# Kernel tuning notes

Hardware: AMD Instinct MI355X
Metric: run time of the kernel (lower is better)

The kernel has to match this reference:

```python
import jax, jax.numpy as jnp
import numpy as np

B, N, D, NS, HID, ITERS = 32, 4096, 256, 8, 128, 3
EPS = 1e-8
LN_EPS = 1e-5


def _ln(x, g, b):
    mu = jnp.mean(x, axis=-1, keepdims=True)
    var = jnp.mean(jnp.square(x - mu), axis=-1, keepdims=True)
    return (x - mu) * jax.lax.rsqrt(var + LN_EPS) * g + b


def setup_inputs() -> dict:
    key = jax.random.key(0)
    ks = jax.random.split(key, 32)
    scale = D ** -0.5

    def lin(k, out_d, in_d):
        return jax.random.normal(k, (out_d, in_d), jnp.float32) * (in_d ** -0.5)

    inp = {
        "inputs": jax.random.normal(ks[0], (B, N, D), jnp.float32),
        "slot_noise": jax.random.normal(ks[1], (B, NS, D), jnp.float32),
        "slots_mu": jax.random.uniform(ks[2], (1, 1, D), jnp.float32, -1.0, 1.0) * scale,
        "slots_sigma": jax.random.uniform(ks[3], (1, 1, D), jnp.float32, -1.0, 1.0) * scale,
        "Wq": lin(ks[4], D, D),
        "Wk": lin(ks[5], D, D),
        "Wv": lin(ks[6], D, D),
        "gru_w_ih": lin(ks[7], 3 * D, 2 * D),
        "gru_w_hh": lin(ks[8], 3 * D, D),
        "gru_b_ih": jnp.zeros((3 * D,), jnp.float32),
        "gru_b_hh": jnp.zeros((3 * D,), jnp.float32),
        "obj_w1": lin(ks[9], HID, D),
        "obj_b1": jnp.zeros((HID,), jnp.float32),
        "obj_w2": lin(ks[10], D, HID),
        "obj_b2": jnp.zeros((D,), jnp.float32),
        "rel_w1": lin(ks[11], HID, 2 * D),
        "rel_b1": jnp.zeros((HID,), jnp.float32),
        "rel_w2": lin(ks[12], D, HID),
        "rel_b2": jnp.zeros((D,), jnp.float32),
        "ln_in_g": jnp.ones((D,), jnp.float32),
        "ln_in_b": jnp.zeros((D,), jnp.float32),
        "ln_s_g": jnp.ones((D,), jnp.float32),
        "ln_s_b": jnp.zeros((D,), jnp.float32),
        "ln_ff_g": jnp.ones((D,), jnp.float32),
        "ln_ff_b": jnp.zeros((D,), jnp.float32),
    }
    return inp


def _rel_msg(x, rel_w1, rel_b1, rel_w2, rel_b2):
    # x: (b, n_s, d). rel_mlp(cat(x_i, x_j)) without materializing the concat:
    # split first layer weight into the x_i and x_j halves.
    A = rel_w1[:, :D]   # (hid, d)
    Bm = rel_w1[:, D:]  # (hid, d)
    xa = jnp.einsum('bid,hd->bih', x, A)
    xb = jnp.einsum('bjd,hd->bjh', x, Bm)
    h = jax.nn.relu(xa[:, :, None, :] + xb[:, None, :, :] + rel_b1)  # (b,ns,ns,hid)
    msg = jnp.einsum('bijh,dh->bijd', h, rel_w2) + rel_b2            # (b,ns,ns,d)
    n_s = x.shape[1]
    diag = jnp.eye(n_s, dtype=bool)[None, :, :, None]
    msg = jnp.where(diag, 0.0, msg)
    return msg.sum(axis=2) / (n_s - 1)


def _gru_cell(x, h, w_ih, w_hh, b_ih, b_hh):
    gx = x @ w_ih.T + b_ih  # (B*, 3d)
    gh = h @ w_hh.T + b_hh
    xr, xz, xn = jnp.split(gx, 3, axis=-1)
    hr, hz, hn = jnp.split(gh, 3, axis=-1)
    r = jax.nn.sigmoid(xr + hr)
    z = jax.nn.sigmoid(xz + hz)
    n = jnp.tanh(xn + r * hn)
    return (1.0 - z) * n + z * h


def reference(inputs, slot_noise, slots_mu, slots_sigma, Wq, Wk, Wv,
              gru_w_ih, gru_w_hh, gru_b_ih, gru_b_hh,
              obj_w1, obj_b1, obj_w2, obj_b2,
              rel_w1, rel_b1, rel_w2, rel_b2,
              ln_in_g, ln_in_b, ln_s_g, ln_s_b, ln_ff_g, ln_ff_b):
    b, n, d = inputs.shape
    n_s = slot_noise.shape[1]
    scale = d ** -0.5

    slots = slots_mu + slot_noise * jnp.exp(slots_sigma)  # (b, n_s, d)

    x = _ln(inputs, ln_in_g, ln_in_b)
    k = jnp.einsum('bnd,ed->bne', x, Wk)
    v = jnp.einsum('bnd,ed->bne', x, Wv)

    attns = []
    for _ in range(ITERS):
        slots_prev = slots
        q = jnp.einsum('bid,ed->bie', _ln(slots, ln_s_g, ln_s_b), Wq)
        dots = jnp.einsum('bid,bjd->bij', q, k) * scale        # (b, n_s, n)
        attn = jax.nn.softmax(dots, axis=1) + EPS              # softmax over slots
        attns.append(attn)
        attn_n = attn / attn.sum(axis=-1, keepdims=True)
        updates = jnp.einsum('bjd,bij->bid', v, attn_n)        # (b, n_s, d)
        rel = _rel_msg(slots_prev, rel_w1, rel_b1, rel_w2, rel_b2)
        gin = jnp.concatenate([updates, rel], axis=-1).reshape(b * n_s, 2 * d)
        slots = _gru_cell(gin, slots_prev.reshape(b * n_s, d),
                          gru_w_ih, gru_w_hh, gru_b_ih, gru_b_hh).reshape(b, n_s, d)
        ff = _ln(slots, ln_ff_g, ln_ff_b)
        slots = slots + (jax.nn.relu(ff @ obj_w1.T + obj_b1) @ obj_w2.T + obj_b2)
    return slots, jnp.stack(attns)
```

## Files before the change

kernel.cpp:

```cpp
#include <hip/hip_runtime.h>
#include <hip/hip_bf16.h>
#include <math.h>

static constexpr int Bc   = 32;
static constexpr int Nc   = 4096;
static constexpr int Dc   = 256;
static constexpr int NSc  = 8;
static constexpr int HIDc = 128;
static constexpr int ITERSc = 3;
#define EPSf 1e-8f
#define LN_EPSf 1e-5f

typedef __attribute__((ext_vector_type(8))) short bf16x8;
typedef __attribute__((ext_vector_type(8))) unsigned short u16x8;
typedef __attribute__((ext_vector_type(4))) float f32x4;

static constexpr int W1AT = 0;
static constexpr int W1BT = 32768;
static constexpr int W2T  = 65536;
static constexpr int OW1T = 98304;
static constexpr int OW2T = 131072;
static constexpr int WHNT = 163840;
static constexpr int TW_ELEMS = 229376;

__device__ __forceinline__ float bf2f(unsigned int u) {
  return __uint_as_float((u & 0xffffu) << 16);
}

__device__ __forceinline__ unsigned short f2bfu(float f) {
  unsigned int u = __float_as_uint(f);
  unsigned int r = (u + 0x7fffu + ((u >> 16) & 1u)) >> 16;
  return (unsigned short)r;
}

__device__ __forceinline__ void gl_lds16(const void* g, void* l) {
  __builtin_amdgcn_global_load_lds(
      (__attribute__((address_space(1))) void*)(g),
      (__attribute__((address_space(3))) void*)(l), 16, 0, 0);
}

__device__ __forceinline__ float block_sum(float v, float* tmp) {
  #pragma unroll
  for (int o = 32; o > 0; o >>= 1) v += __shfl_down(v, o, 64);
  int lane = threadIdx.x & 63, wid = threadIdx.x >> 6;
  __syncthreads();
  if (lane == 0) tmp[wid] = v;
  __syncthreads();
  return tmp[0] + tmp[1] + tmp[2] + tmp[3];
}

__device__ __forceinline__ float sigmf(float x) { return 1.f / (1.f + expf(-x)); }

__global__ __launch_bounds__(256) void k_init_slots(const float* __restrict__ noise,
                                                    const float* __restrict__ mu,
                                                    const float* __restrict__ sigma,
                                                    float* __restrict__ slots) {
  int idx = blockIdx.x * 256 + threadIdx.x;
  int d = idx & (Dc - 1);
  slots[idx] = mu[d] + noise[idx] * expf(sigma[d]);
}

__global__ __launch_bounds__(256) void k_lnx(const float* __restrict__ inp,
                                             const float* __restrict__ lng,
                                             const float* __restrict__ lnb,
                                             unsigned short* __restrict__ X) {
  __shared__ float smu[16], srs[16];
  int t = threadIdx.x, lane = t & 63, w = t >> 6;
  size_t row0 = (size_t)blockIdx.x * 16;
  for (int rr = 0; rr < 4; rr++) {
    int row = w * 4 + rr;
    float4 v = *(const float4*)(inp + (row0 + row) * 256 + lane * 4);
    float s = v.x + v.y + v.z + v.w;
    float q = v.x * v.x + v.y * v.y + v.z * v.z + v.w * v.w;
    #pragma unroll
    for (int o = 32; o > 0; o >>= 1) { s += __shfl_down(s, o, 64); q += __shfl_down(q, o, 64); }
    if (lane == 0) {
      float mu = s * (1.0f / 256.0f);
      smu[row] = mu;
      srs[row] = rsqrtf(q * (1.0f / 256.0f) - mu * mu + LN_EPSf);
    }
  }
  __syncthreads();
  #pragma unroll
  for (int p = 0; p < 2; p++) {
    int idx = p * 256 + t;
    int row = idx >> 5, ch = idx & 31;
    const float* src = inp + (row0 + row) * 256 + ch * 8;
    float mu = smu[row], rs = srs[row];
    float4 x0 = *(const float4*)(src);
    float4 x1 = *(const float4*)(src + 4);
    float4 g0 = *(const float4*)(lng + ch * 8);
    float4 g1 = *(const float4*)(lng + ch * 8 + 4);
    float4 b0 = *(const float4*)(lnb + ch * 8);
    float4 b1 = *(const float4*)(lnb + ch * 8 + 4);
    u16x8 pk;
    pk[0] = f2bfu((x0.x - mu) * rs * g0.x + b0.x);
    pk[1] = f2bfu((x0.y - mu) * rs * g0.y + b0.y);
    pk[2] = f2bfu((x0.z - mu) * rs * g0.z + b0.z);
    pk[3] = f2bfu((x0.w - mu) * rs * g0.w + b0.w);
    pk[4] = f2bfu((x1.x - mu) * rs * g1.x + b1.x);
    pk[5] = f2bfu((x1.y - mu) * rs * g1.y + b1.y);
    pk[6] = f2bfu((x1.z - mu) * rs * g1.z + b1.z);
    pk[7] = f2bfu((x1.w - mu) * rs * g1.w + b1.w);
    *(u16x8*)(X + (row0 + row) * 256 + ch * 8) = pk;
  }
}

__global__ __launch_bounds__(256) void k_wprep(const float* __restrict__ w_ih,
                                               const float* __restrict__ w_hh,
                                               unsigned short* __restrict__ Wcat) {
  int idx = blockIdx.x * 256 + threadIdx.x;
  int o = idx / 768, c = idx - o * 768;
  float v;
  if (c < 512) v = w_ih[o * 512 + c];
  else v = (o < 512) ? w_hh[o * 256 + (c - 512)] : 0.f;
  Wcat[idx] = f2bfu(v);
}

__global__ __launch_bounds__(256) void k_tprep(const float* __restrict__ rel_w1,
                                               const float* __restrict__ rel_w2,
                                               const float* __restrict__ obj_w1,
                                               const float* __restrict__ obj_w2,
                                               const float* __restrict__ w_hh,
                                               unsigned short* __restrict__ Tw) {
  int i = blockIdx.x * 256 + threadIdx.x;
  if (i >= TW_ELEMS) return;
  float v;
  if (i < W1BT) { int j = i - W1AT; int d = j >> 7, h = j & 127; v = rel_w1[h * 512 + d]; }
  else if (i < W2T)  { int j = i - W1BT; int d = j >> 7, h = j & 127; v = rel_w1[h * 512 + 256 + d]; }
  else if (i < OW1T) { int j = i - W2T;  int h = j >> 8, o = j & 255; v = rel_w2[o * 128 + h]; }
  else if (i < OW2T) { int j = i - OW1T; int d = j >> 7, h = j & 127; v = obj_w1[h * 256 + d]; }
  else if (i < WHNT) { int j = i - OW2T; int h = j >> 8, o = j & 255; v = obj_w2[o * 128 + h]; }
  else               { int j = i - WHNT; int d = j >> 8, o = j & 255; v = w_hh[(512 + o) * 256 + d]; }
  Tw[i] = f2bfu(v);
}

__global__ __launch_bounds__(256) void k_mprep(const float* __restrict__ Wk,
                                               const float* __restrict__ Wq,
                                               const float* __restrict__ Wv,
                                               float* __restrict__ MT,
                                               float* __restrict__ WvT) {
  int d = blockIdx.x, t = threadIdx.x;
  float acc = 0.f;
  for (int c = 0; c < 256; c++) acc += Wk[c * 256 + t] * Wq[c * 256 + d];
  MT[d * 256 + t] = acc;
  WvT[d * 256 + t] = Wv[t * 256 + d];
}

__global__ __launch_bounds__(256) void k_qproj0(const float* __restrict__ slots,
                                                const float* __restrict__ MT,
                                                const float* __restrict__ g,
                                                const float* __restrict__ bb_,
                                                unsigned short* __restrict__ qkb,
                                                float* __restrict__ S,
                                                float* __restrict__ updraw) {
  __shared__ float xs[Dc];
  __shared__ float tmp[4];
  int t = threadIdx.x;
  int row = blockIdx.x;
  updraw[row * 256 + t] = 0.f;
  if (blockIdx.x == 0) S[t] = 0.f;
  float x = slots[row * Dc + t];
  float s = block_sum(x, tmp);
  float m = s * (1.0f / Dc);
  float dx = x - m;
  float s2 = block_sum(dx * dx, tmp);
  float rs = rsqrtf(s2 * (1.0f / Dc) + LN_EPSf);
  xs[t] = dx * rs * g[t] + bb_[t];
  __syncthreads();
  float acc = 0.f;
  for (int d = 0; d < 256; d++) acc += MT[d * 256 + t] * xs[d];
  int b = row >> 3, i = row & 7;
  qkb[(size_t)(b * 16 + i) * 256 + t] = f2bfu(acc);
  qkb[(size_t)(b * 16 + 8 + i) * 256 + t] = 0;
}

__global__ __launch_bounds__(256) void k_attn(const unsigned short* __restrict__ qkb,
                                              const unsigned short* __restrict__ X,
                                              float* __restrict__ attn,
                                              float* __restrict__ S,
                                              float* __restrict__ updraw) {
  __shared__ unsigned short xs[64 * 256];
  __shared__ float dots[16][68];
  __shared__ float at[8][64];
  __shared__ float parts[2][8][256];
  int t = threadIdx.x, lane = t & 63, w = t >> 6;
  int b = blockIdx.x >> 6, jc = blockIdx.x & 63;
  int j0 = jc * 64;
  #pragma unroll
  for (int c = 0; c < 8; c++) {
    int slot = c * 256 + t;
    int tok = slot >> 5, sl = slot & 31;
    int gc = (sl & 24) | ((sl & 7) ^ (tok & 7));
    gl_lds16((const char*)X + (((size_t)(b * 4096 + j0 + tok)) * 256 + gc * 8) * 2,
             (char*)xs + (size_t)(c * 256 + w * 64) * 16);
  }
  int m = lane & 15, quad = lane >> 4;
  const unsigned short* qrow = qkb + (size_t)(b * 16 + m) * 256;
  __syncthreads();
  f32x4 dacc = {0.f, 0.f, 0.f, 0.f};
  int tokb = w * 16 + m;
  #pragma unroll
  for (int ks = 0; ks < 8; ks++) {
    bf16x8 afr = *(const bf16x8*)(qrow + ks * 32 + quad * 8);
    int kchunk = ks * 4 + quad;
    int slot = (kchunk & 24) | ((kchunk & 7) ^ (tokb & 7));
    bf16x8 bfr = *(const bf16x8*)((const char*)xs + (size_t)tokb * 512 + slot * 16);
    dacc = __builtin_amdgcn_mfma_f32_16x16x32_bf16(afr, bfr, dacc, 0, 0, 0);
  }
  #pragma unroll
  for (int r = 0; r < 4; r++) dots[quad * 4 + r][tokb] = dacc[r];
  __syncthreads();
  if (t < 64) {
    float a[8], mx = -1e30f;
    #pragma unroll
    for (int i = 0; i < 8; i++) { a[i] = dots[i][t] * 0.0625f; mx = fmaxf(mx, a[i]); }
    float sum = 0.f;
    #pragma unroll
    for (int i = 0; i < 8; i++) { a[i] = expf(a[i] - mx); sum += a[i]; }
    float inv = 1.f / sum;
    float* ab = attn + (size_t)b * NSc * Nc;
    #pragma unroll
    for (int i = 0; i < 8; i++) {
      float v = a[i] * inv + EPSf;
      a[i] = v;
      at[i][t] = v;
      ab[i * Nc + j0 + t] = v;
    }
    #pragma unroll
    for (int i = 0; i < 8; i++) {
      float s = a[i];
      #pragma unroll
      for (int o = 32; o > 0; o >>= 1) s += __shfl_down(s, o, 64);
      if (lane == 0) atomicAdd(&S[b * NSc + i], s);
    }
  }
  __syncthreads();
  int dg = t & 127, h = t >> 7;
  float acc[8][2];
  #pragma unroll
  for (int i = 0; i < 8; i++) { acc[i][0] = 0.f; acc[i][1] = 0.f; }
  int kchunk = dg >> 2;
  for (int jj = 0; jj < 32; jj++) {
    int tok = h * 32 + jj;
    int slot = (kchunk & 24) | ((kchunk & 7) ^ (tok & 7));
    unsigned int xv = *(const unsigned int*)((const char*)xs + (size_t)tok * 512 + slot * 16 + (dg & 3) * 4);
    float x0 = bf2f(xv), x1 = bf2f(xv >> 16);
    #pragma unroll
    for (int i = 0; i < 8; i++) {
      float av = at[i][tok];
      acc[i][0] += av * x0;
      acc[i][1] += av * x1;
    }
  }
  #pragma unroll
  for (int i = 0; i < 8; i++)
    *(float2*)&parts[h][i][dg * 2] = make_float2(acc[i][0], acc[i][1]);
  __syncthreads();
  for (int i = 0; i < 8; i++) {
    float val = parts[0][i][t] + parts[1][i][t];
    atomicAdd(&updraw[(size_t)(b * NSc + i) * 256 + t], val);
  }
}

__global__ __launch_bounds__(256) void k_slot_a(const float* __restrict__ slots,
                                                const float* __restrict__ updraw,
                                                const float* __restrict__ S,
                                                const unsigned short* __restrict__ Tw,
                                                const float* __restrict__ WvT,
                                                const float* __restrict__ b1,
                                                const float* __restrict__ b2,
                                                unsigned short* __restrict__ Xb) {
  __shared__ float sp[NSc][256];
  __shared__ float un[4][256];
  __shared__ float xpart[2][12][128];
  __shared__ float xabl[12][128];
  __shared__ float hs[4][128];
  int t = threadIdx.x;
  int b = blockIdx.x >> 1, half = blockIdx.x & 1;
  int i0 = half * 4;
  for (int x = t; x < NSc * 256; x += 256) sp[x >> 8][x & 255] = slots[b * NSc * 256 + x];
  for (int r = 0; r < 4; r++) {
    int grow = b * NSc + i0 + r;
    un[r][t] = updraw[(size_t)grow * 256 + t] / S[grow];
  }
  __syncthreads();
  {
    float av[4] = {0.f, 0.f, 0.f, 0.f};
    for (int d = 0; d < 256; d++) {
      float wv = WvT[d * 256 + t];
      #pragma unroll
      for (int r = 0; r < 4; r++) av[r] += wv * un[r][d];
    }
    for (int r = 0; r < 4; r++) {
      int grow = b * NSc + i0 + r;
      Xb[(size_t)grow * 768 + t] = f2bfu(av[r]);
      Xb[(size_t)grow * 768 + 512 + t] = f2bfu(sp[i0 + r][t]);
    }
  }
  int h = t & 127, dh = t >> 7;
  {
    const unsigned short* wa = Tw + W1AT;
    const unsigned short* wb = Tw + W1BT;
    float accb[8] = {0, 0, 0, 0, 0, 0, 0, 0};
    float acca[4] = {0, 0, 0, 0};
    for (int dd = 0; dd < 128; dd++) {
      int d = dh * 128 + dd;
      float wbv = bf2f(wb[d * 128 + h]);
      float wav = bf2f(wa[d * 128 + h]);
      #pragma unroll
      for (int jj = 0; jj < 8; jj++) accb[jj] += wbv * sp[jj][d];
      #pragma unroll
      for (int r = 0; r < 4; r++) acca[r] += wav * sp[i0 + r][d];
    }
    #pragma unroll
    for (int jj = 0; jj < 8; jj++) xpart[dh][jj][h] = accb[jj];
    #pragma unroll
    for (int r = 0; r < 4; r++) xpart[dh][8 + r][h] = acca[r];
  }
  __syncthreads();
  {
    int g = t >> 7;
    for (int jj = g * 6; jj < g * 6 + 6; jj++)
      xabl[jj][h] = xpart[0][jj][h] + xpart[1][jj][h];
  }
  __syncthreads();
  {
    float bv = b1[h];
    int ig = t >> 7;
    #pragma unroll
    for (int ii = 0; ii < 2; ii++) {
      int il = ig * 2 + ii;
      int ibatch = i0 + il;
      float av = xabl[8 + il][h];
      float s = 0.f;
      #pragma unroll
      for (int jj = 0; jj < NSc; jj++) {
        if (jj == ibatch) continue;
        s += fmaxf(av + xabl[jj][h] + bv, 0.f);
      }
      hs[il][h] = s;
    }
  }
  __syncthreads();
  {
    const unsigned short* w2 = Tw + W2T;
    float am[4] = {0, 0, 0, 0};
    for (int hh = 0; hh < 128; hh++) {
      float wv = bf2f(w2[hh * 256 + t]);
      #pragma unroll
      for (int r = 0; r < 4; r++) am[r] += wv * hs[r][hh];
    }
    float bv2 = b2[t];
    for (int r = 0; r < 4; r++) {
      float rel = am[r] * (1.0f / 7.0f) + bv2;
      Xb[(size_t)(b * NSc + i0 + r) * 768 + 256 + t] = f2bfu(rel);
    }
  }
}

__global__ __launch_bounds__(256) void k_gates(const unsigned short* __restrict__ Xb,
                                               const unsigned short* __restrict__ Wcat,
                                               unsigned short* __restrict__ Yb) {
  __shared__ unsigned short Als[64 * 64];
  __shared__ unsigned short Bls[64 * 64];
  int tid = threadIdx.x;
  int lane = tid & 63, w = tid >> 6;
  int idx16 = lane & 15, quad = lane >> 4;
  int m0 = (blockIdx.x / 12) * 64;
  int n0 = (blockIdx.x % 12) * 64;
  int wm = w & 1, wn = w >> 1;
  f32x4 acc[2][2];
  #pragma unroll
  for (int i = 0; i < 2; i++)
    #pragma unroll
    for (int j = 0; j < 2; j++) acc[i][j] = (f32x4){0.f, 0.f, 0.f, 0.f};

  for (int kt = 0; kt < 12; kt++) {
    int k0 = kt * 64;
    #pragma unroll
    for (int c = 0; c < 2; c++) {
      int idx = (w * 2 + c) * 64 + lane;
      int row = idx >> 3, lc = idx & 7;
      int gc = lc ^ (row & 7);
      gl_lds16((const char*)Xb + (size_t)(m0 + row) * 1536 + k0 * 2 + gc * 16,
               (char*)Als + (size_t)(w * 2 + c) * 1024);
      gl_lds16((const char*)Wcat + (size_t)(n0 + row) * 1536 + k0 * 2 + gc * 16,
               (char*)Bls + (size_t)(w * 2 + c) * 1024);
    }
    __syncthreads();
    #pragma unroll
    for (int ks = 0; ks < 2; ks++) {
      bf16x8 af[2], bfr[2];
      int kchunk = ks * 4 + quad;
      #pragma unroll
      for (int mt = 0; mt < 2; mt++) {
        int row = wm * 32 + mt * 16 + idx16;
        af[mt] = *(const bf16x8*)((const char*)Als + (size_t)(row * 8 + (kchunk ^ (row & 7))) * 16);
      }
      #pragma unroll
      for (int nt = 0; nt < 2; nt++) {
        int row = wn * 32 + nt * 16 + idx16;
        bfr[nt] = *(const bf16x8*)((const char*)Bls + (size_t)(row * 8 + (kchunk ^ (row & 7))) * 16);
      }
      #pragma unroll
      for (int mt = 0; mt < 2; mt++)
        #pragma unroll
        for (int nt = 0; nt < 2; nt++)
          acc[mt][nt] = __builtin_amdgcn_mfma_f32_16x16x32_bf16(af[mt], bfr[nt], acc[mt][nt], 0, 0, 0);
    }
    __syncthreads();
  }
  #pragma unroll
  for (int mt = 0; mt < 2; mt++) {
    #pragma unroll
    for (int nt = 0; nt < 2; nt++) {
      int gm = m0 + wm * 32 + mt * 16 + quad * 4;
      int col = n0 + wn * 32 + nt * 16 + idx16;
      #pragma unroll
      for (int r = 0; r < 4; r++)
        Yb[(size_t)(gm + r) * 768 + col] = f2bfu(acc[mt][nt][r]);
    }
  }
}

__global__ __launch_bounds__(256) void k_slot_c(const unsigned short* __restrict__ Yb,
                                                const unsigned short* __restrict__ Tw,
                                                const float* __restrict__ MT,
                                                const float* __restrict__ b_ih,
                                                const float* __restrict__ b_hh,
                                                float* __restrict__ slots,
                                                const float* __restrict__ ob1,
                                                const float* __restrict__ ob2,
                                                const float* __restrict__ lng,
                                                const float* __restrict__ lnb,
                                                const float* __restrict__ lsg,
                                                const float* __restrict__ lsb,
                                                unsigned short* __restrict__ qkb,
                                                float* __restrict__ updraw,
                                                float* __restrict__ S,
                                                float* __restrict__ outf,
                                                int wfinal) {
  __shared__ float sp4[4][256];
  __shared__ float ffl[4][256];
  __shared__ float h1p[2][4][128];
  __shared__ float h1l[4][128];
  __shared__ float xs2[4][256];
  int t = threadIdx.x;
  int g0 = blockIdx.x * 4;
  for (int x = t; x < 1024; x += 256) sp4[x >> 8][x & 255] = slots[(size_t)g0 * 256 + x];
  __syncthreads();
  float hn[4] = {0, 0, 0, 0};
  {
    const unsigned short* wh = Tw + WHNT;
    for (int d = 0; d < 256; d++) {
      float wv = bf2f(wh[d * 256 + t]);
      #pragma unroll
      for (int r = 0; r < 4; r++) hn[r] += wv * sp4[r][d];
    }
  }
  float bir = b_ih[t], bhr = b_hh[t];
  float biz = b_ih[256 + t], bhz = b_hh[256 + t];
  float bin_ = b_ih[512 + t], bhn = b_hh[512 + t];
  float snew[4];
  #pragma unroll
  for (int r = 0; r < 4; r++) {
    size_t yoff = (size_t)(g0 + r) * 768;
    float yr = bf2f((unsigned int)Yb[yoff + t]);
    float yz = bf2f((unsigned int)Yb[yoff + 256 + t]);
    float yx = bf2f((unsigned int)Yb[yoff + 512 + t]);
    float rg = sigmf(yr + bir + bhr);
    float zg = sigmf(yz + biz + bhz);
    float ng = tanhf(yx + bin_ + rg * (hn[r] + bhn));
    snew[r] = (1.f - zg) * ng + zg * sp4[r][t];
    ffl[r][t] = snew[r];
  }
  __syncthreads();
  {
    int wv = t >> 6, lane = t & 63;
    float4 v = *(const float4*)&ffl[wv][lane * 4];
    float s = v.x + v.y + v.z + v.w;
    float q = v.x * v.x + v.y * v.y + v.z * v.z + v.w * v.w;
    #pragma unroll
    for (int o = 32; o > 0; o >>= 1) { s += __shfl_down(s, o, 64); q += __shfl_down(q, o, 64); }
    s = __shfl(s, 0, 64); q = __shfl(q, 0, 64);
    float mu = s * (1.0f / 256.0f);
    float rs = rsqrtf(q * (1.0f / 256.0f) - mu * mu + LN_EPSf);
    float4 g4 = *(const float4*)&lng[lane * 4];
    float4 b4 = *(const float4*)&lnb[lane * 4];
    float4 o4;
    o4.x = (v.x - mu) * rs * g4.x + b4.x;
    o4.y = (v.y - mu) * rs * g4.y + b4.y;
    o4.z = (v.z - mu) * rs * g4.z + b4.z;
    o4.w = (v.w - mu) * rs * g4.w + b4.w;
    *(float4*)&ffl[wv][lane * 4] = o4;
  }
  __syncthreads();
  {
    const unsigned short* w1 = Tw + OW1T;
    int h = t & 127, dh = t >> 7;
    float a1[4] = {0, 0, 0, 0};
    for (int dd = 0; dd < 128; dd++) {
      int d = dh * 128 + dd;
      float wv = bf2f(w1[d * 128 + h]);
      #pragma unroll
      for (int r = 0; r < 4; r++) a1[r] += wv * ffl[r][d];
    }
    #pragma unroll
    for (int r = 0; r < 4; r++) h1p[dh][r][h] = a1[r];
  }
  __syncthreads();
  {
    int h = t & 127, g = t >> 7;
    float bo = ob1[h];
    #pragma unroll
    for (int rr = 0; rr < 2; rr++) {
      int r = g * 2 + rr;
      h1l[r][h] = fmaxf(h1p[0][r][h] + h1p[1][r][h] + bo, 0.f);
    }
  }
  __syncthreads();
  float res[4];
  {
    const unsigned short* w2 = Tw + OW2T;
    float ao[4] = {0, 0, 0, 0};
    for (int hh = 0; hh < 128; hh++) {
      float wv = bf2f(w2[hh * 256 + t]);
      #pragma unroll
      for (int r = 0; r < 4; r++) ao[r] += wv * h1l[r][hh];
    }
    float bo2 = ob2[t];
    #pragma unroll
    for (int r = 0; r < 4; r++) res[r] = snew[r] + ao[r] + bo2;
  }
  #pragma unroll
  for (int r = 0; r < 4; r++) {
    slots[(size_t)(g0 + r) * 256 + t] = res[r];
    if (wfinal) outf[(size_t)(g0 + r) * 256 + t] = res[r];
    xs2[r][t] = res[r];
  }
  __syncthreads();
  {
    int wv = t >> 6, lane = t & 63;
    float4 v = *(const float4*)&xs2[wv][lane * 4];
    float s = v.x + v.y + v.z + v.w;
    float q = v.x * v.x + v.y * v.y + v.z * v.z + v.w * v.w;
    #pragma unroll
    for (int o = 32; o > 0; o >>= 1) { s += __shfl_down(s, o, 64); q += __shfl_down(q, o, 64); }
    s = __shfl(s, 0, 64); q = __shfl(q, 0, 64);
    float mu = s * (1.0f / 256.0f);
    float rs = rsqrtf(q * (1.0f / 256.0f) - mu * mu + LN_EPSf);
    float4 g4 = *(const float4*)&lsg[lane * 4];
    float4 b4 = *(const float4*)&lsb[lane * 4];
    float4 o4;
    o4.x = (v.x - mu) * rs * g4.x + b4.x;
    o4.y = (v.y - mu) * rs * g4.y + b4.y;
    o4.z = (v.z - mu) * rs * g4.z + b4.z;
    o4.w = (v.w - mu) * rs * g4.w + b4.w;
    *(float4*)&xs2[wv][lane * 4] = o4;
  }
  __syncthreads();
  {
    float aq[4] = {0, 0, 0, 0};
    for (int d = 0; d < 256; d++) {
      float wv = MT[d * 256 + t];
      #pragma unroll
      for (int r = 0; r < 4; r++) aq[r] += wv * xs2[r][d];
    }
    #pragma unroll
    for (int r = 0; r < 4; r++) {
      int grow = g0 + r;
      int b = grow >> 3, i = grow & 7;
      qkb[(size_t)(b * 16 + i) * 256 + t] = f2bfu(aq[r]);
      qkb[(size_t)(b * 16 + 8 + i) * 256 + t] = 0;
    }
  }
  #pragma unroll
  for (int r = 0; r < 4; r++) updraw[(size_t)(g0 + r) * 256 + t] = 0.f;
  if (t < 4) S[g0 + t] = 0.f;
}

extern "C" void kernel_launch(void* const* d_in, const int* in_sizes, int n_in,
                              void* d_out, int out_size, void* d_ws, size_t ws_size,
                              hipStream_t stream) {
  const float* inputs      = (const float*)d_in[0];
  const float* slot_noise  = (const float*)d_in[1];
  const float* slots_mu    = (const float*)d_in[2];
  const float* slots_sigma = (const float*)d_in[3];
  const float* Wq          = (const float*)d_in[4];
  const float* Wk          = (const float*)d_in[5];
  const float* Wv          = (const float*)d_in[6];
  const float* gru_w_ih    = (const float*)d_in[7];
  const float* gru_w_hh    = (const float*)d_in[8];
  const float* gru_b_ih    = (const float*)d_in[9];
  const float* gru_b_hh    = (const float*)d_in[10];
  const float* obj_w1      = (const float*)d_in[11];
  const float* obj_b1      = (const float*)d_in[12];
  const float* obj_w2      = (const float*)d_in[13];
  const float* obj_b2      = (const float*)d_in[14];
  const float* rel_w1      = (const float*)d_in[15];
  const float* rel_b1      = (const float*)d_in[16];
  const float* rel_w2      = (const float*)d_in[17];
  const float* rel_b2      = (const float*)d_in[18];
  const float* ln_in_g     = (const float*)d_in[19];
  const float* ln_in_b     = (const float*)d_in[20];
  const float* ln_s_g      = (const float*)d_in[21];
  const float* ln_s_b      = (const float*)d_in[22];
  const float* ln_ff_g     = (const float*)d_in[23];
  const float* ln_ff_b     = (const float*)d_in[24];

  char* w = (char*)d_ws;
  unsigned short* X    = (unsigned short*)(w);
  float* slots  = (float*)(w + (size_t)67108864);
  float* updraw = (float*)(w + (size_t)67371008);
  float* Sbuf   = (float*)(w + (size_t)67633152);
  unsigned short* Wcat = (unsigned short*)(w + (size_t)67634176);
  unsigned short* Tw   = (unsigned short*)(w + (size_t)68813824);
  unsigned short* Xbuf = (unsigned short*)(w + (size_t)69403648);
  unsigned short* Ybuf = (unsigned short*)(w + (size_t)69796864);
  unsigned short* qkb  = (unsigned short*)(w + (size_t)70190080);
  float* MT  = (float*)(w + (size_t)70452224);
  float* WvT = (float*)(w + (size_t)70714368);

  float* out = (float*)d_out;
  float* attn_base = out + (size_t)Bc * NSc * Dc;

  k_init_slots<<<Bc * NSc * Dc / 256, 256, 0, stream>>>(slot_noise, slots_mu, slots_sigma, slots);
  k_lnx<<<Bc * Nc / 16, 256, 0, stream>>>(inputs, ln_in_g, ln_in_b, X);
  k_wprep<<<768 * 768 / 256, 256, 0, stream>>>(gru_w_ih, gru_w_hh, Wcat);
  k_tprep<<<(TW_ELEMS + 255) / 256, 256, 0, stream>>>(rel_w1, rel_w2, obj_w1, obj_w2, gru_w_hh, Tw);
  k_mprep<<<256, 256, 0, stream>>>(Wk, Wq, Wv, MT, WvT);
  k_qproj0<<<Bc * NSc, 256, 0, stream>>>(slots, MT, ln_s_g, ln_s_b, qkb, Sbuf, updraw);

  for (int it = 0; it < ITERSc; it++) {
    float* attn = attn_base + (size_t)it * Bc * NSc * Nc;
    k_attn<<<Bc * 64, 256, 0, stream>>>(qkb, X, attn, Sbuf, updraw);
    k_slot_a<<<Bc * 2, 256, 0, stream>>>(slots, updraw, Sbuf, Tw, WvT, rel_b1, rel_b2, Xbuf);
    k_gates<<<4 * 12, 256, 0, stream>>>(Xbuf, Wcat, Ybuf);
    k_slot_c<<<64, 256, 0, stream>>>(Ybuf, Tw, MT, gru_b_ih, gru_b_hh, slots,
                                     obj_b1, obj_b2, ln_ff_g, ln_ff_b, ln_s_g, ln_s_b,
                                     qkb, updraw, Sbuf,
                                     out, it == ITERSc - 1 ? 1 : 0);
  }
}
```

Measured before the change: 798.3 us.

## Move attention update product onto MFMA using a pre-transposed bf16 input copy

The LayerNorm kernel now also writes a token-major transposed bf16 copy of the normalized inputs. The attention kernel is rewritten with far fewer, larger blocks: each wave computes dots via MFMA straight from global memory and does the 8-slot softmax with lane shuffles. It then computes the attention-weighted value sum with MFMA against the transposed copy, replacing the scalar LDS accumulation loop. Smaller changes: the padded q buffer is dropped, the zero block of the GRU weight matrix is skipped by splitting it in two, and the MT/WvT matrices are stored in bf16. This costs an extra 64MB transposed write, lower occupancy, and slightly lower precision.

```diff
diff --git a/kernel.cpp b/kernel.cpp
--- a/kernel.cpp
+++ b/kernel.cpp
@@ -63,12 +63,16 @@
 __global__ __launch_bounds__(256) void k_lnx(const float* __restrict__ inp,
                                              const float* __restrict__ lng,
                                              const float* __restrict__ lnb,
-                                             unsigned short* __restrict__ X) {
-  __shared__ float smu[16], srs[16];
+                                             unsigned short* __restrict__ X,
+                                             unsigned short* __restrict__ XT) {
+  __shared__ float smu[64], srs[64];
+  __shared__ unsigned short xt[64][264];
   int t = threadIdx.x, lane = t & 63, w = t >> 6;
-  size_t row0 = (size_t)blockIdx.x * 16;
-  for (int rr = 0; rr < 4; rr++) {
-    int row = w * 4 + rr;
+  int b = blockIdx.x >> 6;
+  int tok0 = (blockIdx.x & 63) * 64;
+  size_t row0 = (size_t)b * 4096 + tok0;
+  for (int rr = 0; rr < 16; rr++) {
+    int row = w * 16 + rr;
     float4 v = *(const float4*)(inp + (row0 + row) * 256 + lane * 4);
     float s = v.x + v.y + v.z + v.w;
     float q = v.x * v.x + v.y * v.y + v.z * v.z + v.w * v.w;
@@ -82,7 +86,7 @@
   }
   __syncthreads();
   #pragma unroll
-  for (int p = 0; p < 2; p++) {
+  for (int p = 0; p < 8; p++) {
     int idx = p * 256 + t;
     int row = idx >> 5, ch = idx & 31;
     const float* src = inp + (row0 + row) * 256 + ch * 8;
@@ -103,18 +107,35 @@
     pk[6] = f2bfu((x1.z - mu) * rs * g1.z + b1.z);
     pk[7] = f2bfu((x1.w - mu) * rs * g1.w + b1.w);
     *(u16x8*)(X + (row0 + row) * 256 + ch * 8) = pk;
+    *(u16x8*)&xt[row][ch * 8] = pk;
+  }
+  __syncthreads();
+  {
+    unsigned short* dst = XT + ((size_t)(b * 256 + t)) * 4096 + tok0;
+    #pragma unroll
+    for (int g = 0; g < 8; g++) {
+      u16x8 o;
+      #pragma unroll
+      for (int u = 0; u < 8; u++) o[u] = xt[g * 8 + u][t];
+      *(u16x8*)(dst + g * 8) = o;
+    }
   }
 }
 
 __global__ __launch_bounds__(256) void k_wprep(const float* __restrict__ w_ih,
                                                const float* __restrict__ w_hh,
-                                               unsigned short* __restrict__ Wcat) {
+                                               unsigned short* __restrict__ Wcat1,
+                                               unsigned short* __restrict__ Wcat2) {
   int idx = blockIdx.x * 256 + threadIdx.x;
-  int o = idx / 768, c = idx - o * 768;
-  float v;
-  if (c < 512) v = w_ih[o * 512 + c];
-  else v = (o < 512) ? w_hh[o * 256 + (c - 512)] : 0.f;
-  Wcat[idx] = f2bfu(v);
+  if (idx < 512 * 768) {
+    int o = idx / 768, c = idx - o * 768;
+    float v = (c < 512) ? w_ih[o * 512 + c] : w_hh[o * 256 + (c - 512)];
+    Wcat1[idx] = f2bfu(v);
+  } else {
+    int j = idx - 512 * 768;
+    int o = j >> 9, c = j & 511;
+    Wcat2[j] = f2bfu(w_ih[(512 + o) * 512 + c]);
+  }
 }
 
 __global__ __launch_bounds__(256) void k_tprep(const float* __restrict__ rel_w1,
@@ -138,17 +159,17 @@
 __global__ __launch_bounds__(256) void k_mprep(const float* __restrict__ Wk,
                                                const float* __restrict__ Wq,
                                                const float* __restrict__ Wv,
-                                               float* __restrict__ MT,
-                                               float* __restrict__ WvT) {
+                                               unsigned short* __restrict__ MTb,
+                                               unsigned short* __restrict__ WvTb) {
   int d = blockIdx.x, t = threadIdx.x;
   float acc = 0.f;
   for (int c = 0; c < 256; c++) acc += Wk[c * 256 + t] * Wq[c * 256 + d];
-  MT[d * 256 + t] = acc;
-  WvT[d * 256 + t] = Wv[t * 256 + d];
+  MTb[d * 256 + t] = f2bfu(acc);
+  WvTb[d * 256 + t] = f2bfu(Wv[t * 256 + d]);
 }
 
 __global__ __launch_bounds__(256) void k_qproj0(const float* __restrict__ slots,
-                                                const float* __restrict__ MT,
+                                                const unsigned short* __restrict__ MTb,
                                                 const float* __restrict__ g,
                                                 const float* __restrict__ bb_,
                                                 unsigned short* __restrict__ qkb,
@@ -169,97 +190,104 @@
   xs[t] = dx * rs * g[t] + bb_[t];
   __syncthreads();
   float acc = 0.f;
-  for (int d = 0; d < 256; d++) acc += MT[d * 256 + t] * xs[d];
-  int b = row >> 3, i = row & 7;
-  qkb[(size_t)(b * 16 + i) * 256 + t] = f2bfu(acc);
-  qkb[(size_t)(b * 16 + 8 + i) * 256 + t] = 0;
+  for (int d = 0; d < 256; d++) acc += bf2f(MTb[d * 256 + t]) * xs[d];
+  qkb[(size_t)row * 256 + t] = f2bfu(acc);
 }
 
 __global__ __launch_bounds__(256) void k_attn(const unsigned short* __restrict__ qkb,
                                               const unsigned short* __restrict__ X,
+                                              const unsigned short* __restrict__ XT,
                                               float* __restrict__ attn,
                                               float* __restrict__ S,
                                               float* __restrict__ updraw) {
-  __shared__ unsigned short xs[64 * 256];
-  __shared__ float dots[16][68];
-  __shared__ float at[8][64];
-  __shared__ float parts[2][8][256];
+  __shared__ unsigned short at_bf[4][16][136];
+  __shared__ float updw[4][8][256];
   int t = threadIdx.x, lane = t & 63, w = t >> 6;
-  int b = blockIdx.x >> 6, jc = blockIdx.x & 63;
-  int j0 = jc * 64;
-  #pragma unroll
-  for (int c = 0; c < 8; c++) {
-    int slot = c * 256 + t;
-    int tok = slot >> 5, sl = slot & 31;
-    int gc = (sl & 24) | ((sl & 7) ^ (tok & 7));
-    gl_lds16((const char*)X + (((size_t)(b * 4096 + j0 + tok)) * 256 + gc * 8) * 2,
-             (char*)xs + (size_t)(c * 256 + w * 64) * 16);
-  }
-  int m = lane & 15, quad = lane >> 4;
-  const unsigned short* qrow = qkb + (size_t)(b * 16 + m) * 256;
-  __syncthreads();
-  f32x4 dacc = {0.f, 0.f, 0.f, 0.f};
-  int tokb = w * 16 + m;
-  #pragma unroll
-  for (int ks = 0; ks < 8; ks++) {
-    bf16x8 afr = *(const bf16x8*)(qrow + ks * 32 + quad * 8);
-    int kchunk = ks * 4 + quad;
-    int slot = (kchunk & 24) | ((kchunk & 7) ^ (tokb & 7));
-    bf16x8 bfr = *(const bf16x8*)((const char*)xs + (size_t)tokb * 512 + slot * 16);
-    dacc = __builtin_amdgcn_mfma_f32_16x16x32_bf16(afr, bfr, dacc, 0, 0, 0);
-  }
-  #pragma unroll
-  for (int r = 0; r < 4; r++) dots[quad * 4 + r][tokb] = dacc[r];
-  __syncthreads();
-  if (t < 64) {
-    float a[8], mx = -1e30f;
-    #pragma unroll
-    for (int i = 0; i < 8; i++) { a[i] = dots[i][t] * 0.0625f; mx = fmaxf(mx, a[i]); }
-    float sum = 0.f;
-    #pragma unroll
-    for (int i = 0; i < 8; i++) { a[i] = expf(a[i] - mx); sum += a[i]; }
-    float inv = 1.f / sum;
-    float* ab = attn + (size_t)b * NSc * Nc;
-    #pragma unroll
-    for (int i = 0; i < 8; i++) {
-      float v = a[i] * inv + EPSf;
-      a[i] = v;
-      at[i][t] = v;
-      ab[i * Nc + j0 + t] = v;
-    }
-    #pragma unroll
-    for (int i = 0; i < 8; i++) {
-      float s = a[i];
-      #pragma unroll
-      for (int o = 32; o > 0; o >>= 1) s += __shfl_down(s, o, 64);
-      if (lane == 0) atomicAdd(&S[b * NSc + i], s);
-    }
-  }
-  __syncthreads();
-  int dg = t & 127, h = t >> 7;
-  float acc[8][2];
-  #pragma unroll
-  for (int i = 0; i < 8; i++) { acc[i][0] = 0.f; acc[i][1] = 0.f; }
-  int kchunk = dg >> 2;
-  for (int jj = 0; jj < 32; jj++) {
-    int tok = h * 32 + jj;
-    int slot = (kchunk & 24) | ((kchunk & 7) ^ (tok & 7));
-    unsigned int xv = *(const unsigned int*)((const char*)xs + (size_t)tok * 512 + slot * 16 + (dg & 3) * 4);
-    float x0 = bf2f(xv), x1 = bf2f(xv >> 16);
-    #pragma unroll
-    for (int i = 0; i < 8; i++) {
-      float av = at[i][tok];
-      acc[i][0] += av * x0;
-      acc[i][1] += av * x1;
-    }
-  }
-  #pragma unroll
-  for (int i = 0; i < 8; i++)
-    *(float2*)&parts[h][i][dg * 2] = make_float2(acc[i][0], acc[i][1]);
+  int b = blockIdx.x >> 3, chunk = blockIdx.x & 7;
+  int n = lane & 15, quad = lane >> 4;
+  int tokbase = chunk * 512 + w * 128;
+  {
+    unsigned int* z = (unsigned int*)&at_bf[w][8][0];
+    for (int i = lane; i < 544 / 2 * 2 / 2; i += 64) z[i] = 0;
+  }
+  {
+    unsigned int* z = (unsigned int*)&at_bf[w][8][0];
+    for (int i = lane; i < 544; i += 64) z[i] = 0u;
+  }
+  const unsigned short* qrow = qkb + ((size_t)(b * 8 + (n & 7))) * 256 + quad * 8;
+  const unsigned short* xbase = X + ((size_t)(b * 4096 + tokbase + n)) * 256 + quad * 8;
+  bf16x8 zz;
+  #pragma unroll
+  for (int u = 0; u < 8; u++) zz[u] = 0;
+  float sacc[4] = {0.f, 0.f, 0.f, 0.f};
+  for (int tt = 0; tt < 8; tt++) {
+    f32x4 dacc = {0.f, 0.f, 0.f, 0.f};
+    const unsigned short* xrow = xbase + (size_t)(tt * 16) * 256;
+    #pragma unroll
+    for (int ks = 0; ks < 8; ks++) {
+      bf16x8 afr = *(const bf16x8*)(qrow + ks * 32);
+      if (n >= 8) afr = zz;
+      bf16x8 bfr = *(const bf16x8*)(xrow + ks * 32);
+      dacc = __builtin_amdgcn_mfma_f32_16x16x32_bf16(afr, bfr, dacc, 0, 0, 0);
+    }
+    float v[4], p[4];
+    #pragma unroll
+    for (int r = 0; r < 4; r++) v[r] = dacc[r] * 0.0625f;
+    #pragma unroll
+    for (int r = 0; r < 4; r++) p[r] = __shfl_xor(v[r], 16, 64);
+    float mx = fmaxf(fmaxf(fmaxf(v[0], v[1]), fmaxf(v[2], v[3])),
+                     fmaxf(fmaxf(p[0], p[1]), fmaxf(p[2], p[3])));
+    float e[4], se = 0.f;
+    #pragma unroll
+    for (int r = 0; r < 4; r++) { e[r] = expf(v[r] - mx); se += e[r]; }
+    float so = __shfl_xor(se, 16, 64);
+    float inv = 1.f / (se + so);
+    if (lane < 32) {
+      float* ab = attn + (size_t)b * NSc * Nc + (size_t)(quad * 4) * Nc + (tokbase + tt * 16 + n);
+      #pragma unroll
+      for (int r = 0; r < 4; r++) {
+        float a = e[r] * inv + EPSf;
+        sacc[r] += a;
+        ab[(size_t)r * Nc] = a;
+        at_bf[w][quad * 4 + r][tt * 16 + n] = f2bfu(a);
+      }
+    }
+  }
+  if (lane < 32) {
+    #pragma unroll
+    for (int r = 0; r < 4; r++) {
+      float s = sacc[r];
+      s += __shfl_xor(s, 1, 64);
+      s += __shfl_xor(s, 2, 64);
+      s += __shfl_xor(s, 4, 64);
+      s += __shfl_xor(s, 8, 64);
+      if (n == 0) atomicAdd(&S[b * NSc + quad * 4 + r], s);
+    }
+  }
+  bf16x8 afr[4];
+  #pragma unroll
+  for (int kk = 0; kk < 4; kk++)
+    afr[kk] = *(const bf16x8*)&at_bf[w][n][kk * 32 + quad * 8];
+  const unsigned short* xtb = XT + ((size_t)(b * 256 + n)) * 4096 + tokbase + quad * 8;
+  #pragma unroll
+  for (int nt = 0; nt < 16; nt++) {
+    f32x4 pacc = {0.f, 0.f, 0.f, 0.f};
+    const unsigned short* xr = xtb + (size_t)(nt * 16) * 4096;
+    #pragma unroll
+    for (int kk = 0; kk < 4; kk++) {
+      bf16x8 bfr = *(const bf16x8*)(xr + kk * 32);
+      pacc = __builtin_amdgcn_mfma_f32_16x16x32_bf16(afr[kk], bfr, pacc, 0, 0, 0);
+    }
+    if (lane < 32) {
+      #pragma unroll
+      for (int r = 0; r < 4; r++)
+        updw[w][quad * 4 + r][nt * 16 + n] = pacc[r];
+    }
+  }
   __syncthreads();
   for (int i = 0; i < 8; i++) {
-    float val = parts[0][i][t] + parts[1][i][t];
-    atomicAdd(&updraw[(size_t)(b * NSc + i) * 256 + t], val);
+    float s = updw[0][i][t] + updw[1][i][t] + updw[2][i][t] + updw[3][i][t];
+    atomicAdd(&updraw[(size_t)(b * NSc + i) * 256 + t], s);
   }
 }
 
@@ -267,7 +295,7 @@
                                                 const float* __restrict__ updraw,
                                                 const float* __restrict__ S,
                                                 const unsigned short* __restrict__ Tw,
-                                                const float* __restrict__ WvT,
+                                                const unsigned short* __restrict__ WvTb,
                                                 const float* __restrict__ b1,
                                                 const float* __restrict__ b2,
                                                 unsigned short* __restrict__ Xb) {
@@ -288,7 +316,7 @@
   {
     float av[4] = {0.f, 0.f, 0.f, 0.f};
     for (int d = 0; d < 256; d++) {
-      float wv = WvT[d * 256 + t];
+      float wv = bf2f(WvTb[d * 256 + t]);
       #pragma unroll
       for (int r = 0; r < 4; r++) av[r] += wv * un[r][d];
     }
@@ -360,15 +388,22 @@
 }
 
 __global__ __launch_bounds__(256) void k_gates(const unsigned short* __restrict__ Xb,
-                                               const unsigned short* __restrict__ Wcat,
+                                               const unsigned short* __restrict__ Wcat1,
+                                               const unsigned short* __restrict__ Wcat2,
                                                unsigned short* __restrict__ Yb) {
   __shared__ unsigned short Als[64 * 64];
   __shared__ unsigned short Bls[64 * 64];
   int tid = threadIdx.x;
   int lane = tid & 63, w = tid >> 6;
   int idx16 = lane & 15, quad = lane >> 4;
-  int m0 = (blockIdx.x / 12) * 64;
-  int n0 = (blockIdx.x % 12) * 64;
+  int mt6 = blockIdx.x / 12, ntile = blockIdx.x % 12;
+  int m0 = mt6 * 64;
+  int n0 = ntile * 64;
+  const unsigned short* wb;
+  int ktm;
+  size_t rowbytes;
+  if (ntile < 8) { wb = Wcat1 + (size_t)n0 * 768; ktm = 12; rowbytes = 1536; }
+  else { wb = Wcat2 + (size_t)(ntile - 8) * 64 * 512; ktm = 8; rowbytes = 1024; }
   int wm = w & 1, wn = w >> 1;
   f32x4 acc[2][2];
   #pragma unroll
@@ -376,7 +411,7 @@
     #pragma unroll
     for (int j = 0; j < 2; j++) acc[i][j] = (f32x4){0.f, 0.f, 0.f, 0.f};
 
-  for (int kt = 0; kt < 12; kt++) {
+  for (int kt = 0; kt < ktm; kt++) {
     int k0 = kt * 64;
     #pragma unroll
     for (int c = 0; c < 2; c++) {
@@ -385,7 +420,7 @@
       int gc = lc ^ (row & 7);
       gl_lds16((const char*)Xb + (size_t)(m0 + row) * 1536 + k0 * 2 + gc * 16,
                (char*)Als + (size_t)(w * 2 + c) * 1024);
-      gl_lds16((const char*)Wcat + (size_t)(n0 + row) * 1536 + k0 * 2 + gc * 16,
+      gl_lds16((const char*)wb + (size_t)row * rowbytes + k0 * 2 + gc * 16,
                (char*)Bls + (size_t)(w * 2 + c) * 1024);
     }
     __syncthreads();
@@ -426,7 +461,7 @@
 
 __global__ __launch_bounds__(256) void k_slot_c(const unsigned short* __restrict__ Yb,
                                                 const unsigned short* __restrict__ Tw,
-                                                const float* __restrict__ MT,
+                                                const unsigned short* __restrict__ MTb,
                                                 const float* __restrict__ b_ih,
                                                 const float* __restrict__ b_hh,
                                                 float* __restrict__ slots,
@@ -563,17 +598,13 @@
   {
     float aq[4] = {0, 0, 0, 0};
     for (int d = 0; d < 256; d++) {
-      float wv = MT[d * 256 + t];
+      float wv = bf2f(MTb[d * 256 + t]);
       #pragma unroll
       for (int r = 0; r < 4; r++) aq[r] += wv * xs2[r][d];
     }
     #pragma unroll
-    for (int r = 0; r < 4; r++) {
-      int grow = g0 + r;
-      int b = grow >> 3, i = grow & 7;
-      qkb[(size_t)(b * 16 + i) * 256 + t] = f2bfu(aq[r]);
-      qkb[(size_t)(b * 16 + 8 + i) * 256 + t] = 0;
-    }
+    for (int r = 0; r < 4; r++)
+      qkb[(size_t)(g0 + r) * 256 + t] = f2bfu(aq[r]);
   }
   #pragma unroll
   for (int r = 0; r < 4; r++) updraw[(size_t)(g0 + r) * 256 + t] = 0.f;
@@ -610,34 +641,36 @@
   const float* ln_ff_b     = (const float*)d_in[24];
 
   char* w = (char*)d_ws;
-  unsigned short* X    = (unsigned short*)(w);
-  float* slots  = (float*)(w + (size_t)67108864);
-  float* updraw = (float*)(w + (size_t)67371008);
-  float* Sbuf   = (float*)(w + (size_t)67633152);
-  unsigned short* Wcat = (unsigned short*)(w + (size_t)67634176);
-  unsigned short* Tw   = (unsigned short*)(w + (size_t)68813824);
-  unsigned short* Xbuf = (unsigned short*)(w + (size_t)69403648);
-  unsigned short* Ybuf = (unsigned short*)(w + (size_t)69796864);
-  unsigned short* qkb  = (unsigned short*)(w + (size_t)70190080);
-  float* MT  = (float*)(w + (size_t)70452224);
-  float* WvT = (float*)(w + (size_t)70714368);
+  unsigned short* X  = (unsigned short*)(w);
+  unsigned short* XT = (unsigned short*)(w + (size_t)67108864);
+  float* slots  = (float*)(w + (size_t)134217728);
+  float* updraw = (float*)(w + (size_t)134479872);
+  float* Sbuf   = (float*)(w + (size_t)134742016);
+  unsigned short* Wcat1 = (unsigned short*)(w + (size_t)134743040);
+  unsigned short* Wcat2 = (unsigned short*)(w + (size_t)135529472);
+  unsigned short* Tw    = (unsigned short*)(w + (size_t)135791616);
+  unsigned short* MTb   = (unsigned short*)(w + (size_t)136250368);
+  unsigned short* WvTb  = (unsigned short*)(w + (size_t)136381440);
+  unsigned short* Xbuf  = (unsigned short*)(w + (size_t)136512512);
+  unsigned short* qkb   = (unsigned short*)(w + (size_t)136512512);
+  unsigned short* Ybuf  = (unsigned short*)(w + (size_t)136905728);
 
   float* out = (float*)d_out;
   float* attn_base = out + (size_t)Bc * NSc * Dc;
 
   k_init_slots<<<Bc * NSc * Dc / 256, 256, 0, stream>>>(slot_noise, slots_mu, slots_sigma, slots);
-  k_lnx<<<Bc * Nc / 16, 256, 0, stream>>>(inputs, ln_in_g, ln_in_b, X);
-  k_wprep<<<768 * 768 / 256, 256, 0, stream>>>(gru_w_ih, gru_w_hh, Wcat);
+  k_lnx<<<Bc * 64, 256, 0, stream>>>(inputs, ln_in_g, ln_in_b, X, XT);
+  k_wprep<<<(512 * 768 + 256 * 512) / 256, 256, 0, stream>>>(gru_w_ih, gru_w_hh, Wcat1, Wcat2);
   k_tprep<<<(TW_ELEMS + 255) / 256, 256, 0, stream>>>(rel_w1, rel_w2, obj_w1, obj_w2, gru_w_hh, Tw);
-  k_mprep<<<256, 256, 0, stream>>>(Wk, Wq, Wv, MT, WvT);
-  k_qproj0<<<Bc * NSc, 256, 0, stream>>>(slots, MT, ln_s_g, ln_s_b, qkb, Sbuf, updraw);
+  k_mprep<<<256, 256, 0, stream>>>(Wk, Wq, Wv, MTb, WvTb);
+  k_qproj0<<<Bc * NSc, 256, 0, stream>>>(slots, MTb, ln_s_g, ln_s_b, qkb, Sbuf, updraw);
 
   for (int it = 0; it < ITERSc; it++) {
     float* attn = attn_base + (size_t)it * Bc * NSc * Nc;
-    k_attn<<<Bc * 64, 256, 0, stream>>>(qkb, X, attn, Sbuf, updraw);
-    k_slot_a<<<Bc * 2, 256, 0, stream>>>(slots, updraw, Sbuf, Tw, WvT, rel_b1, rel_b2, Xbuf);
-    k_gates<<<4 * 12, 256, 0, stream>>>(Xbuf, Wcat, Ybuf);
-    k_slot_c<<<64, 256, 0, stream>>>(Ybuf, Tw, MT, gru_b_ih, gru_b_hh, slots,
+    k_attn<<<Bc * 8, 256, 0, stream>>>(qkb, X, XT, attn, Sbuf, updraw);
+    k_slot_a<<<Bc * 2, 256, 0, stream>>>(slots, updraw, Sbuf, Tw, WvTb, rel_b1, rel_b2, Xbuf);
+    k_gates<<<4 * 12, 256, 0, stream>>>(Xbuf, Wcat1, Wcat2, Ybuf);
+    k_slot_c<<<64, 256, 0, stream>>>(Ybuf, Tw, MTb, gru_b_ih, gru_b_hh, slots,
                                      obj_b1, obj_b2, ln_ff_g, ln_ff_b, ln_s_g, ln_s_b,
                                      qkb, updraw, Sbuf,
                                      out, it == ITERSc - 1 ? 1 : 0);
```

After: 665.9 us. -16.6%, faster.
